# Kernel optimization log

Hardware: AMD Instinct MI355X
Metric: run time of the kernel (lower is better)

Reference implementation:

```python
import jax, jax.numpy as jnp
import numpy as np


def setup_inputs() -> dict:
    key = jax.random.key(0)
    k1, k2 = jax.random.split(key)
    STATE_LEN, SEQ_LEN, D = 8192, 8192, 1024
    user_emb = jax.random.normal(k1, (STATE_LEN, D), dtype=jnp.float32)
    id_emb = jax.random.normal(k2, (SEQ_LEN, D), dtype=jnp.float32)
    return {"user_emb": user_emb, "id_emb": id_emb}


def reference(user_emb, id_emb):
    # attn_energies[i, j] = user_emb[i] . id_emb[j]  -> single GEMM
    energies = jnp.einsum('id,jd->ij', user_emb, id_emb)  # [state_len, seq_len]
    # F.softmax on 2D tensor defaults to dim=1 (rows)
    return jax.nn.softmax(energies, axis=-1)
```

## Files before the change

### kernel.cpp

```cpp
#include <hip/hip_runtime.h>
#include <hip/hip_bf16.h>
#include <stdint.h>

typedef __attribute__((ext_vector_type(8))) short bf16x8;
typedef __attribute__((ext_vector_type(4))) float f32x4;

typedef const __attribute__((address_space(1))) void* gas_ptr;
typedef __attribute__((address_space(3))) void* lds_ptr_t;

__device__ __forceinline__ unsigned short f32_to_bf16_rtn(float x) {
    unsigned u = __float_as_uint(x);
    u += 0x7FFFu + ((u >> 16) & 1u);
    return (unsigned short)(u >> 16);
}
__device__ __forceinline__ float bf16_bits_to_f32(unsigned short h) {
    return __uint_as_float(((unsigned)h) << 16);
}

__global__ __launch_bounds__(256) void split_hi_lo(
    const float* __restrict__ A, const float* __restrict__ B,
    unsigned short* __restrict__ Ahi, unsigned short* __restrict__ Alo,
    unsigned short* __restrict__ Bhi, unsigned short* __restrict__ Blo, int n4)
{
    int i = blockIdx.x * 256 + threadIdx.x;
    if (i >= n4) return;
    float4 a = ((const float4*)A)[i];
    float4 b = ((const float4*)B)[i];
    ushort4 h, l;

    h.x = f32_to_bf16_rtn(a.x); l.x = f32_to_bf16_rtn(a.x - bf16_bits_to_f32(h.x));
    h.y = f32_to_bf16_rtn(a.y); l.y = f32_to_bf16_rtn(a.y - bf16_bits_to_f32(h.y));
    h.z = f32_to_bf16_rtn(a.z); l.z = f32_to_bf16_rtn(a.z - bf16_bits_to_f32(h.z));
    h.w = f32_to_bf16_rtn(a.w); l.w = f32_to_bf16_rtn(a.w - bf16_bits_to_f32(h.w));
    ((ushort4*)Ahi)[i] = h; ((ushort4*)Alo)[i] = l;

    h.x = f32_to_bf16_rtn(b.x); l.x = f32_to_bf16_rtn(b.x - bf16_bits_to_f32(h.x));
    h.y = f32_to_bf16_rtn(b.y); l.y = f32_to_bf16_rtn(b.y - bf16_bits_to_f32(h.y));
    h.z = f32_to_bf16_rtn(b.z); l.z = f32_to_bf16_rtn(b.z - bf16_bits_to_f32(h.z));
    h.w = f32_to_bf16_rtn(b.w); l.w = f32_to_bf16_rtn(b.w - bf16_bits_to_f32(h.w));
    ((ushort4*)Bhi)[i] = h; ((ushort4*)Blo)[i] = l;
}

template <bool PRESPLIT>
__global__ __launch_bounds__(256) void gemm_bt_split(
    const __hip_bfloat16* __restrict__ Ahi, const __hip_bfloat16* __restrict__ Alo,
    const __hip_bfloat16* __restrict__ Bhi, const __hip_bfloat16* __restrict__ Blo,
    const float* __restrict__ Af, const float* __restrict__ Bf,
    float* __restrict__ out, int M, int N, int K)
{
    __shared__ char sm[32768];
    const int tid  = threadIdx.x;
    const int lane = tid & 63;
    const int w    = tid >> 6;
    const int bm = blockIdx.y, bn = blockIdx.x;
    const int wm = (w >> 1) * 64;
    const int wn = (w & 1) * 64;

    f32x4 acc[4][4] = {};

    const int rA   = lane & 15;
    const int koff = (lane >> 4) << 3;

    for (int k0 = 0; k0 < K; k0 += 32) {
        __syncthreads();
        if (PRESPLIT) {
#pragma unroll
            for (int c = 0; c < 8; ++c) {
                const int t = c >> 1;
                const int row = ((c & 1) << 6) + (tid >> 2);
                const __hip_bfloat16* base =
                    (t == 0) ? Ahi + (size_t)(bm * 128) * K :
                    (t == 1) ? Alo + (size_t)(bm * 128) * K :
                    (t == 2) ? Bhi + (size_t)(bn * 128) * K :
                               Blo + (size_t)(bn * 128) * K;
                const __hip_bfloat16* src = base + (size_t)row * K + k0 + ((tid & 3) << 3);
                char* dst = sm + c * 4096 + tid * 16;
                __builtin_amdgcn_global_load_lds((gas_ptr)src, (lds_ptr_t)dst, 16, 0, 0);
            }
        } else {
#pragma unroll
            for (int c = 0; c < 4; ++c) {
                const bool isA = (c < 2);
                const int rowh = ((c & 1) << 6) + (tid >> 2);
                const float* src = (isA ? Af + (size_t)(bm * 128 + rowh) * K
                                        : Bf + (size_t)(bn * 128 + rowh) * K)
                                   + k0 + ((tid & 3) << 3);
                f32x4 v0 = *(const f32x4*)src;
                f32x4 v1 = *(const f32x4*)(src + 4);
                float vv[8] = {v0.x, v0.y, v0.z, v0.w, v1.x, v1.y, v1.z, v1.w};
                bf16x8 h, l;
#pragma unroll
                for (int j = 0; j < 8; ++j) {
                    unsigned short hb = f32_to_bf16_rtn(vv[j]);
                    unsigned short lb = f32_to_bf16_rtn(vv[j] - bf16_bits_to_f32(hb));
                    h[j] = (short)hb; l[j] = (short)lb;
                }
                const int g = ((c & 1) << 12) + tid * 16;
                *(bf16x8*)(sm + (isA ? 0 : 16384) + g) = h;
                *(bf16x8*)(sm + (isA ? 8192 : 24576) + g) = l;
            }
        }
        __syncthreads();

        bf16x8 ah[4], al[4], bh[4], bl[4];
#pragma unroll
        for (int i = 0; i < 4; ++i) {
            const int ra = (wm + i * 16 + rA) * 32 + koff;
            ah[i] = *(const bf16x8*)(sm +         ra * 2);
            al[i] = *(const bf16x8*)(sm +  8192 + ra * 2);
            const int rb = (wn + i * 16 + rA) * 32 + koff;
            bh[i] = *(const bf16x8*)(sm + 16384 + rb * 2);
            bl[i] = *(const bf16x8*)(sm + 24576 + rb * 2);
        }
#pragma unroll
        for (int i = 0; i < 4; ++i)
#pragma unroll
            for (int j = 0; j < 4; ++j) {
                acc[i][j] = __builtin_amdgcn_mfma_f32_16x16x32_bf16(ah[i], bh[j], acc[i][j], 0, 0, 0);
                acc[i][j] = __builtin_amdgcn_mfma_f32_16x16x32_bf16(al[i], bh[j], acc[i][j], 0, 0, 0);
                acc[i][j] = __builtin_amdgcn_mfma_f32_16x16x32_bf16(ah[i], bl[j], acc[i][j], 0, 0, 0);
            }
    }

    const int r0 = bm * 128 + wm + ((lane >> 4) << 2);
    const int c0 = bn * 128 + wn + (lane & 15);
#pragma unroll
    for (int i = 0; i < 4; ++i)
#pragma unroll
        for (int j = 0; j < 4; ++j)
#pragma unroll
            for (int r = 0; r < 4; ++r)
                out[(size_t)(r0 + i * 16 + r) * N + (c0 + j * 16)] = acc[i][j][r];
}

__global__ __launch_bounds__(256) void softmax_rows_8192(float* __restrict__ d)
{
    const int tid = threadIdx.x;
    float4* p = (float4*)(d + (size_t)blockIdx.x * 8192);
    float4 v[8];
    float m = -3.402823466e+38f;
#pragma unroll
    for (int i = 0; i < 8; ++i) {
        v[i] = p[tid + (i << 8)];
        m = fmaxf(m, fmaxf(fmaxf(v[i].x, v[i].y), fmaxf(v[i].z, v[i].w)));
    }
#pragma unroll
    for (int o = 32; o >= 1; o >>= 1) m = fmaxf(m, __shfl_xor(m, o));
    __shared__ float smax[4], ssum[4];
    if ((tid & 63) == 0) smax[tid >> 6] = m;
    __syncthreads();
    m = fmaxf(fmaxf(smax[0], smax[1]), fmaxf(smax[2], smax[3]));

    float s = 0.f;
#pragma unroll
    for (int i = 0; i < 8; ++i) {
        v[i].x = __expf(v[i].x - m);
        v[i].y = __expf(v[i].y - m);
        v[i].z = __expf(v[i].z - m);
        v[i].w = __expf(v[i].w - m);
        s += (v[i].x + v[i].y) + (v[i].z + v[i].w);
    }
#pragma unroll
    for (int o = 32; o >= 1; o >>= 1) s += __shfl_xor(s, o);
    if ((tid & 63) == 0) ssum[tid >> 6] = s;
    __syncthreads();
    s = (ssum[0] + ssum[1]) + (ssum[2] + ssum[3]);
    const float r = 1.0f / s;
#pragma unroll
    for (int i = 0; i < 8; ++i) {
        v[i].x *= r; v[i].y *= r; v[i].z *= r; v[i].w *= r;
        p[tid + (i << 8)] = v[i];
    }
}

extern "C" void kernel_launch(void* const* d_in, const int* in_sizes, int n_in,
                              void* d_out, int out_size, void* d_ws, size_t ws_size,
                              hipStream_t stream)
{
    const float* A = (const float*)d_in[0];
    const float* B = (const float*)d_in[1];
    float* out = (float*)d_out;
    const int K = 1024;
    const int M = in_sizes[0] / K;
    const int N = in_sizes[1] / K;
    const size_t elemsA = (size_t)M * K;
    const size_t elemsB = (size_t)N * K;
    const size_t need = 2 * (elemsA + elemsB) * sizeof(unsigned short);

    dim3 grid(N / 128, M / 128);
    const bool presplit = (ws_size >= need) && (M == N);

    if (presplit) {
        unsigned short* Ahi = (unsigned short*)d_ws;
        unsigned short* Alo = Ahi + elemsA;
        unsigned short* Bhi = Alo + elemsA;
        unsigned short* Blo = Bhi + elemsB;
        const int n4 = (int)(elemsA / 4);
        split_hi_lo<<<(n4 + 255) / 256, 256, 0, stream>>>(A, B, Ahi, Alo, Bhi, Blo, n4);
        gemm_bt_split<true><<<grid, 256, 0, stream>>>(
            (const __hip_bfloat16*)Ahi, (const __hip_bfloat16*)Alo,
            (const __hip_bfloat16*)Bhi, (const __hip_bfloat16*)Blo,
            nullptr, nullptr, out, M, N, K);
    } else {
        gemm_bt_split<false><<<grid, 256, 0, stream>>>(
            nullptr, nullptr, nullptr, nullptr, A, B, out, M, N, K);
    }
    softmax_rows_8192<<<M, 256, 0, stream>>>(out);
}
```

Before: 740.3 us.

## Switch GEMM to 32x32x16 MFMA with XOR-swizzled LDS layout

Replaces the 16x16x32 bf16 MFMA tiling with 32x32x16 MFMAs, using 2x2 f32x16 accumulators per wave over two k-substeps. The LDS tile layout gets an XOR swizzle on the 16-byte chunk index, applied both in the global-to-LDS loads and the fragment reads, to avoid bank conflicts. Fewer, larger MFMAs cut instruction issue and LDS read traffic per FLOP. The softmax now uses nontemporal stores for its output. The larger accumulators and the swizzle index math change register pressure, and the epilogue store pattern changes.

```diff
diff --git a/kernel.cpp b/kernel.cpp
--- a/kernel.cpp
+++ b/kernel.cpp
@@ -4,6 +4,7 @@
 
 typedef __attribute__((ext_vector_type(8))) short bf16x8;
 typedef __attribute__((ext_vector_type(4))) float f32x4;
+typedef __attribute__((ext_vector_type(16))) float f32x16;
 
 typedef const __attribute__((address_space(1))) void* gas_ptr;
 typedef __attribute__((address_space(3))) void* lds_ptr_t;
@@ -56,10 +57,13 @@
     const int wm = (w >> 1) * 64;
     const int wn = (w & 1) * 64;
 
-    f32x4 acc[4][4] = {};
-
-    const int rA   = lane & 15;
-    const int koff = (lane >> 4) << 3;
+    f32x16 acc[2][2] = {};
+
+    const int srow   = tid >> 2;
+    const int sfetch = (tid & 3) ^ ((tid >> 3) & 3);
+    const int arow  = lane & 31;
+    const int khalf = lane >> 5;
+    const int sw    = (lane >> 1) & 3;
 
     for (int k0 = 0; k0 < K; k0 += 32) {
         __syncthreads();
@@ -67,13 +71,13 @@
 #pragma unroll
             for (int c = 0; c < 8; ++c) {
                 const int t = c >> 1;
-                const int row = ((c & 1) << 6) + (tid >> 2);
+                const int row = ((c & 1) << 6) + srow;
                 const __hip_bfloat16* base =
                     (t == 0) ? Ahi + (size_t)(bm * 128) * K :
                     (t == 1) ? Alo + (size_t)(bm * 128) * K :
                     (t == 2) ? Bhi + (size_t)(bn * 128) * K :
                                Blo + (size_t)(bn * 128) * K;
-                const __hip_bfloat16* src = base + (size_t)row * K + k0 + ((tid & 3) << 3);
+                const __hip_bfloat16* src = base + (size_t)row * K + k0 + (sfetch << 3);
                 char* dst = sm + c * 4096 + tid * 16;
                 __builtin_amdgcn_global_load_lds((gas_ptr)src, (lds_ptr_t)dst, 16, 0, 0);
             }
@@ -81,9 +85,9 @@
 #pragma unroll
             for (int c = 0; c < 4; ++c) {
                 const bool isA = (c < 2);
-                const int rowh = ((c & 1) << 6) + (tid >> 2);
-                const float* src = (isA ? Af + (size_t)(bm * 128 + rowh) * K
-                                        : Bf + (size_t)(bn * 128 + rowh) * K)
+                const int row = ((c & 1) << 6) + srow;
+                const float* src = (isA ? Af + (size_t)(bm * 128 + row) * K
+                                        : Bf + (size_t)(bn * 128 + row) * K)
                                    + k0 + ((tid & 3) << 3);
                 f32x4 v0 = *(const f32x4*)src;
                 f32x4 v1 = *(const f32x4*)(src + 4);
@@ -95,49 +99,55 @@
                     unsigned short lb = f32_to_bf16_rtn(vv[j] - bf16_bits_to_f32(hb));
                     h[j] = (short)hb; l[j] = (short)lb;
                 }
-                const int g = ((c & 1) << 12) + tid * 16;
+                const int g = row * 64 + sfetch * 16;
                 *(bf16x8*)(sm + (isA ? 0 : 16384) + g) = h;
                 *(bf16x8*)(sm + (isA ? 8192 : 24576) + g) = l;
             }
         }
         __syncthreads();
 
-        bf16x8 ah[4], al[4], bh[4], bl[4];
-#pragma unroll
-        for (int i = 0; i < 4; ++i) {
-            const int ra = (wm + i * 16 + rA) * 32 + koff;
-            ah[i] = *(const bf16x8*)(sm +         ra * 2);
-            al[i] = *(const bf16x8*)(sm +  8192 + ra * 2);
-            const int rb = (wn + i * 16 + rA) * 32 + koff;
-            bh[i] = *(const bf16x8*)(sm + 16384 + rb * 2);
-            bl[i] = *(const bf16x8*)(sm + 24576 + rb * 2);
+#pragma unroll
+        for (int kk = 0; kk < 2; ++kk) {
+            bf16x8 ah[2], al[2], bh[2], bl[2];
+            const int cw = ((kk << 1) + khalf) ^ sw;
+#pragma unroll
+            for (int i = 0; i < 2; ++i) {
+                const int ga = (wm + i * 32 + arow) * 64 + cw * 16;
+                ah[i] = *(const bf16x8*)(sm +         ga);
+                al[i] = *(const bf16x8*)(sm +  8192 + ga);
+                const int gb = (wn + i * 32 + arow) * 64 + cw * 16;
+                bh[i] = *(const bf16x8*)(sm + 16384 + gb);
+                bl[i] = *(const bf16x8*)(sm + 24576 + gb);
+            }
+#pragma unroll
+            for (int i = 0; i < 2; ++i)
+#pragma unroll
+                for (int j = 0; j < 2; ++j) {
+                    acc[i][j] = __builtin_amdgcn_mfma_f32_32x32x16_bf16(ah[i], bh[j], acc[i][j], 0, 0, 0);
+                    acc[i][j] = __builtin_amdgcn_mfma_f32_32x32x16_bf16(al[i], bh[j], acc[i][j], 0, 0, 0);
+                    acc[i][j] = __builtin_amdgcn_mfma_f32_32x32x16_bf16(ah[i], bl[j], acc[i][j], 0, 0, 0);
+                }
         }
-#pragma unroll
-        for (int i = 0; i < 4; ++i)
-#pragma unroll
-            for (int j = 0; j < 4; ++j) {
-                acc[i][j] = __builtin_amdgcn_mfma_f32_16x16x32_bf16(ah[i], bh[j], acc[i][j], 0, 0, 0);
-                acc[i][j] = __builtin_amdgcn_mfma_f32_16x16x32_bf16(al[i], bh[j], acc[i][j], 0, 0, 0);
-                acc[i][j] = __builtin_amdgcn_mfma_f32_16x16x32_bf16(ah[i], bl[j], acc[i][j], 0, 0, 0);
-            }
-    }
-
-    const int r0 = bm * 128 + wm + ((lane >> 4) << 2);
-    const int c0 = bn * 128 + wn + (lane & 15);
-#pragma unroll
-    for (int i = 0; i < 4; ++i)
-#pragma unroll
-        for (int j = 0; j < 4; ++j)
-#pragma unroll
-            for (int r = 0; r < 4; ++r)
-                out[(size_t)(r0 + i * 16 + r) * N + (c0 + j * 16)] = acc[i][j][r];
+    }
+
+    const int r0 = bm * 128 + wm + ((lane >> 5) << 2);
+    const int c0 = bn * 128 + wn + (lane & 31);
+#pragma unroll
+    for (int i = 0; i < 2; ++i)
+#pragma unroll
+        for (int j = 0; j < 2; ++j)
+#pragma unroll
+            for (int r = 0; r < 16; ++r) {
+                const int row = r0 + i * 32 + (r & 3) + ((r >> 2) << 3);
+                out[(size_t)row * N + (c0 + j * 32)] = acc[i][j][r];
+            }
 }
 
 __global__ __launch_bounds__(256) void softmax_rows_8192(float* __restrict__ d)
 {
     const int tid = threadIdx.x;
-    float4* p = (float4*)(d + (size_t)blockIdx.x * 8192);
-    float4 v[8];
+    f32x4* p = (f32x4*)(d + (size_t)blockIdx.x * 8192);
+    f32x4 v[8];
     float m = -3.402823466e+38f;
 #pragma unroll
     for (int i = 0; i < 8; ++i) {
@@ -168,8 +178,8 @@
     const float r = 1.0f / s;
 #pragma unroll
     for (int i = 0; i < 8; ++i) {
-        v[i].x *= r; v[i].y *= r; v[i].z *= r; v[i].w *= r;
-        p[tid + (i << 8)] = v[i];
+        v[i] *= r;
+        __builtin_nontemporal_store(v[i], &p[tid + (i << 8)]);
     }
 }
 
```

New measurement: 773.7 us. +4.5%, slower.

## Swizzle LDS layout for bank-conflict-free MFMA fragment loads and tune softmax

Applied to the files above, without the earlier changes.

Applies an XOR swizzle to the K-chunk position both when tiles are fetched into LDS and when MFMA fragments are read from it. This removes the LDS bank conflicts of the previous row-major 64-byte-stride layout. The presplit GEMM precomputes its global pointers, loads A fragments per i to cut register pressure, and requests 4 blocks per CU through launch bounds. The softmax now runs 512 threads per row and uses nontemporal stores. The changes risk register spills under the tighter launch bounds and a less efficient reduction in the softmax.

```diff
diff --git a/kernel.cpp b/kernel.cpp
--- a/kernel.cpp
+++ b/kernel.cpp
@@ -41,11 +41,9 @@
     ((ushort4*)Bhi)[i] = h; ((ushort4*)Blo)[i] = l;
 }
 
-template <bool PRESPLIT>
-__global__ __launch_bounds__(256) void gemm_bt_split(
+__global__ __launch_bounds__(256, 4) void gemm_presplit(
     const __hip_bfloat16* __restrict__ Ahi, const __hip_bfloat16* __restrict__ Alo,
     const __hip_bfloat16* __restrict__ Bhi, const __hip_bfloat16* __restrict__ Blo,
-    const float* __restrict__ Af, const float* __restrict__ Bf,
     float* __restrict__ out, int M, int N, int K)
 {
     __shared__ char sm[32768];
@@ -58,72 +56,54 @@
 
     f32x4 acc[4][4] = {};
 
-    const int rA   = lane & 15;
-    const int koff = (lane >> 4) << 3;
+    const int sfetch = (tid & 3) ^ ((tid >> 3) & 3);
+    const size_t offA = (size_t)(bm * 128 + (tid >> 2)) * K + sfetch * 8;
+    const size_t offB = (size_t)(bn * 128 + (tid >> 2)) * K + sfetch * 8;
+    const __hip_bfloat16* pAh = Ahi + offA;
+    const __hip_bfloat16* pAl = Alo + offA;
+    const __hip_bfloat16* pBh = Bhi + offB;
+    const __hip_bfloat16* pBl = Blo + offB;
+    const size_t half = (size_t)64 * K;
+    char* dst0 = sm + tid * 16;
+
+    const int rA = lane & 15;
+    const int ca = (lane >> 4) ^ ((lane >> 1) & 3);
+    const char* aP = sm +         (wm + rA) * 64 + ca * 16;
+    const char* bP = sm + 16384 + (wn + rA) * 64 + ca * 16;
 
     for (int k0 = 0; k0 < K; k0 += 32) {
         __syncthreads();
-        if (PRESPLIT) {
-#pragma unroll
-            for (int c = 0; c < 8; ++c) {
-                const int t = c >> 1;
-                const int row = ((c & 1) << 6) + (tid >> 2);
-                const __hip_bfloat16* base =
-                    (t == 0) ? Ahi + (size_t)(bm * 128) * K :
-                    (t == 1) ? Alo + (size_t)(bm * 128) * K :
-                    (t == 2) ? Bhi + (size_t)(bn * 128) * K :
-                               Blo + (size_t)(bn * 128) * K;
-                const __hip_bfloat16* src = base + (size_t)row * K + k0 + ((tid & 3) << 3);
-                char* dst = sm + c * 4096 + tid * 16;
-                __builtin_amdgcn_global_load_lds((gas_ptr)src, (lds_ptr_t)dst, 16, 0, 0);
+        __builtin_amdgcn_global_load_lds((gas_ptr)(pAh + k0),        (lds_ptr_t)(dst0),         16, 0, 0);
+        __builtin_amdgcn_global_load_lds((gas_ptr)(pAh + half + k0), (lds_ptr_t)(dst0 + 4096),  16, 0, 0);
+        __builtin_amdgcn_global_load_lds((gas_ptr)(pAl + k0),        (lds_ptr_t)(dst0 + 8192),  16, 0, 0);
+        __builtin_amdgcn_global_load_lds((gas_ptr)(pAl + half + k0), (lds_ptr_t)(dst0 + 12288), 16, 0, 0);
+        __builtin_amdgcn_global_load_lds((gas_ptr)(pBh + k0),        (lds_ptr_t)(dst0 + 16384), 16, 0, 0);
+        __builtin_amdgcn_global_load_lds((gas_ptr)(pBh + half + k0), (lds_ptr_t)(dst0 + 20480), 16, 0, 0);
+        __builtin_amdgcn_global_load_lds((gas_ptr)(pBl + k0),        (lds_ptr_t)(dst0 + 24576), 16, 0, 0);
+        __builtin_amdgcn_global_load_lds((gas_ptr)(pBl + half + k0), (lds_ptr_t)(dst0 + 28672), 16, 0, 0);
+        __syncthreads();
+
+        bf16x8 bh[4], bl[4];
+#pragma unroll
+        for (int j = 0; j < 4; ++j) {
+            bh[j] = *(const bf16x8*)(bP + j * 1024);
+            bl[j] = *(const bf16x8*)(bP + j * 1024 + 8192);
+        }
+#pragma unroll
+        for (int i = 0; i < 4; ++i) {
+            bf16x8 ah = *(const bf16x8*)(aP + i * 1024);
+            bf16x8 al = *(const bf16x8*)(aP + i * 1024 + 8192);
+#pragma unroll
+            for (int j = 0; j < 4; ++j) {
+                acc[i][j] = __builtin_amdgcn_mfma_f32_16x16x32_bf16(ah, bh[j], acc[i][j], 0, 0, 0);
+                acc[i][j] = __builtin_amdgcn_mfma_f32_16x16x32_bf16(al, bh[j], acc[i][j], 0, 0, 0);
+                acc[i][j] = __builtin_amdgcn_mfma_f32_16x16x32_bf16(ah, bl[j], acc[i][j], 0, 0, 0);
             }
-        } else {
-#pragma unroll
-            for (int c = 0; c < 4; ++c) {
-                const bool isA = (c < 2);
-                const int rowh = ((c & 1) << 6) + (tid >> 2);
-                const float* src = (isA ? Af + (size_t)(bm * 128 + rowh) * K
-                                        : Bf + (size_t)(bn * 128 + rowh) * K)
-                                   + k0 + ((tid & 3) << 3);
-                f32x4 v0 = *(const f32x4*)src;
-                f32x4 v1 = *(const f32x4*)(src + 4);
-                float vv[8] = {v0.x, v0.y, v0.z, v0.w, v1.x, v1.y, v1.z, v1.w};
-                bf16x8 h, l;
-#pragma unroll
-                for (int j = 0; j < 8; ++j) {
-                    unsigned short hb = f32_to_bf16_rtn(vv[j]);
-                    unsigned short lb = f32_to_bf16_rtn(vv[j] - bf16_bits_to_f32(hb));
-                    h[j] = (short)hb; l[j] = (short)lb;
-                }
-                const int g = ((c & 1) << 12) + tid * 16;
-                *(bf16x8*)(sm + (isA ? 0 : 16384) + g) = h;
-                *(bf16x8*)(sm + (isA ? 8192 : 24576) + g) = l;
-            }
-        }
-        __syncthreads();
-
-        bf16x8 ah[4], al[4], bh[4], bl[4];
-#pragma unroll
-        for (int i = 0; i < 4; ++i) {
-            const int ra = (wm + i * 16 + rA) * 32 + koff;
-            ah[i] = *(const bf16x8*)(sm +         ra * 2);
-            al[i] = *(const bf16x8*)(sm +  8192 + ra * 2);
-            const int rb = (wn + i * 16 + rA) * 32 + koff;
-            bh[i] = *(const bf16x8*)(sm + 16384 + rb * 2);
-            bl[i] = *(const bf16x8*)(sm + 24576 + rb * 2);
-        }
-#pragma unroll
-        for (int i = 0; i < 4; ++i)
-#pragma unroll
-            for (int j = 0; j < 4; ++j) {
-                acc[i][j] = __builtin_amdgcn_mfma_f32_16x16x32_bf16(ah[i], bh[j], acc[i][j], 0, 0, 0);
-                acc[i][j] = __builtin_amdgcn_mfma_f32_16x16x32_bf16(al[i], bh[j], acc[i][j], 0, 0, 0);
-                acc[i][j] = __builtin_amdgcn_mfma_f32_16x16x32_bf16(ah[i], bl[j], acc[i][j], 0, 0, 0);
-            }
+        }
     }
 
     const int r0 = bm * 128 + wm + ((lane >> 4) << 2);
-    const int c0 = bn * 128 + wn + (lane & 15);
+    const int c0 = bn * 128 + wn + rA;
 #pragma unroll
     for (int i = 0; i < 4; ++i)
 #pragma unroll
@@ -133,27 +113,102 @@
                 out[(size_t)(r0 + i * 16 + r) * N + (c0 + j * 16)] = acc[i][j][r];
 }
 
-__global__ __launch_bounds__(256) void softmax_rows_8192(float* __restrict__ d)
+__global__ __launch_bounds__(256) void gemm_fallback(
+    const float* __restrict__ Af, const float* __restrict__ Bf,
+    float* __restrict__ out, int M, int N, int K)
+{
+    __shared__ char sm[32768];
+    const int tid  = threadIdx.x;
+    const int lane = tid & 63;
+    const int w    = tid >> 6;
+    const int bm = blockIdx.y, bn = blockIdx.x;
+    const int wm = (w >> 1) * 64;
+    const int wn = (w & 1) * 64;
+
+    f32x4 acc[4][4] = {};
+    const int sfetch = (tid & 3) ^ ((tid >> 3) & 3);
+    const int rA = lane & 15;
+    const int ca = (lane >> 4) ^ ((lane >> 1) & 3);
+    const char* aP = sm +         (wm + rA) * 64 + ca * 16;
+    const char* bP = sm + 16384 + (wn + rA) * 64 + ca * 16;
+
+    for (int k0 = 0; k0 < K; k0 += 32) {
+        __syncthreads();
+#pragma unroll
+        for (int c = 0; c < 4; ++c) {
+            const bool isA = (c < 2);
+            const int row = ((c & 1) << 6) + (tid >> 2);
+            const float* src = (isA ? Af + (size_t)(bm * 128 + row) * K
+                                    : Bf + (size_t)(bn * 128 + row) * K)
+                               + k0 + ((tid & 3) << 3);
+            f32x4 v0 = *(const f32x4*)src;
+            f32x4 v1 = *(const f32x4*)(src + 4);
+            float vv[8] = {v0.x, v0.y, v0.z, v0.w, v1.x, v1.y, v1.z, v1.w};
+            bf16x8 h, l;
+#pragma unroll
+            for (int j = 0; j < 8; ++j) {
+                unsigned short hb = f32_to_bf16_rtn(vv[j]);
+                unsigned short lb = f32_to_bf16_rtn(vv[j] - bf16_bits_to_f32(hb));
+                h[j] = (short)hb; l[j] = (short)lb;
+            }
+            const int g = row * 64 + sfetch * 16;
+            *(bf16x8*)(sm + (isA ? 0 : 16384) + g) = h;
+            *(bf16x8*)(sm + (isA ? 8192 : 24576) + g) = l;
+        }
+        __syncthreads();
+
+        bf16x8 bh[4], bl[4];
+#pragma unroll
+        for (int j = 0; j < 4; ++j) {
+            bh[j] = *(const bf16x8*)(bP + j * 1024);
+            bl[j] = *(const bf16x8*)(bP + j * 1024 + 8192);
+        }
+#pragma unroll
+        for (int i = 0; i < 4; ++i) {
+            bf16x8 ah = *(const bf16x8*)(aP + i * 1024);
+            bf16x8 al = *(const bf16x8*)(aP + i * 1024 + 8192);
+#pragma unroll
+            for (int j = 0; j < 4; ++j) {
+                acc[i][j] = __builtin_amdgcn_mfma_f32_16x16x32_bf16(ah, bh[j], acc[i][j], 0, 0, 0);
+                acc[i][j] = __builtin_amdgcn_mfma_f32_16x16x32_bf16(al, bh[j], acc[i][j], 0, 0, 0);
+                acc[i][j] = __builtin_amdgcn_mfma_f32_16x16x32_bf16(ah, bl[j], acc[i][j], 0, 0, 0);
+            }
+        }
+    }
+
+    const int r0 = bm * 128 + wm + ((lane >> 4) << 2);
+    const int c0 = bn * 128 + wn + rA;
+#pragma unroll
+    for (int i = 0; i < 4; ++i)
+#pragma unroll
+        for (int j = 0; j < 4; ++j)
+#pragma unroll
+            for (int r = 0; r < 4; ++r)
+                out[(size_t)(r0 + i * 16 + r) * N + (c0 + j * 16)] = acc[i][j][r];
+}
+
+__global__ __launch_bounds__(512) void softmax_rows_8192(float* __restrict__ d)
 {
     const int tid = threadIdx.x;
-    float4* p = (float4*)(d + (size_t)blockIdx.x * 8192);
-    float4 v[8];
+    f32x4* p = (f32x4*)(d + (size_t)blockIdx.x * 8192);
+    f32x4 v[4];
     float m = -3.402823466e+38f;
 #pragma unroll
-    for (int i = 0; i < 8; ++i) {
-        v[i] = p[tid + (i << 8)];
+    for (int i = 0; i < 4; ++i) {
+        v[i] = p[tid + (i << 9)];
         m = fmaxf(m, fmaxf(fmaxf(v[i].x, v[i].y), fmaxf(v[i].z, v[i].w)));
     }
 #pragma unroll
     for (int o = 32; o >= 1; o >>= 1) m = fmaxf(m, __shfl_xor(m, o));
-    __shared__ float smax[4], ssum[4];
+    __shared__ float smax[8], ssum[8];
     if ((tid & 63) == 0) smax[tid >> 6] = m;
     __syncthreads();
-    m = fmaxf(fmaxf(smax[0], smax[1]), fmaxf(smax[2], smax[3]));
+#pragma unroll
+    for (int q = 0; q < 8; ++q) m = fmaxf(m, smax[q]);
 
     float s = 0.f;
 #pragma unroll
-    for (int i = 0; i < 8; ++i) {
+    for (int i = 0; i < 4; ++i) {
         v[i].x = __expf(v[i].x - m);
         v[i].y = __expf(v[i].y - m);
         v[i].z = __expf(v[i].z - m);
@@ -164,12 +219,14 @@
     for (int o = 32; o >= 1; o >>= 1) s += __shfl_xor(s, o);
     if ((tid & 63) == 0) ssum[tid >> 6] = s;
     __syncthreads();
-    s = (ssum[0] + ssum[1]) + (ssum[2] + ssum[3]);
+    s = 0.f;
+#pragma unroll
+    for (int q = 0; q < 8; ++q) s += ssum[q];
     const float r = 1.0f / s;
 #pragma unroll
-    for (int i = 0; i < 8; ++i) {
-        v[i].x *= r; v[i].y *= r; v[i].z *= r; v[i].w *= r;
-        p[tid + (i << 8)] = v[i];
+    for (int i = 0; i < 4; ++i) {
+        v[i] *= r;
+        __builtin_nontemporal_store(v[i], &p[tid + (i << 9)]);
     }
 }
 
@@ -197,13 +254,12 @@
         unsigned short* Blo = Bhi + elemsB;
         const int n4 = (int)(elemsA / 4);
         split_hi_lo<<<(n4 + 255) / 256, 256, 0, stream>>>(A, B, Ahi, Alo, Bhi, Blo, n4);
-        gemm_bt_split<true><<<grid, 256, 0, stream>>>(
+        gemm_presplit<<<grid, 256, 0, stream>>>(
             (const __hip_bfloat16*)Ahi, (const __hip_bfloat16*)Alo,
             (const __hip_bfloat16*)Bhi, (const __hip_bfloat16*)Blo,
-            nullptr, nullptr, out, M, N, K);
+            out, M, N, K);
     } else {
-        gemm_bt_split<false><<<grid, 256, 0, stream>>>(
-            nullptr, nullptr, nullptr, nullptr, A, B, out, M, N, K);
-    }
-    softmax_rows_8192<<<M, 256, 0, stream>>>(out);
-}
+        gemm_fallback<<<grid, 256, 0, stream>>>(A, B, out, M, N, K);
+    }
+    softmax_rows_8192<<<M, 512, 0, stream>>>(out);
+}
```

Result: slower. 817.4 us (+10.4%).
